# Kernel optimization log

Hardware: AMD Instinct MI355X
Metric: run time of the kernel (lower is better)

The kernel has to match this reference:

```python
import jax, jax.numpy as jnp
import numpy as np

B, D, E, K, H = 16384, 4096, 64, 8, 128


def setup_inputs() -> dict:
    key = jax.random.key(0)
    ks = jax.random.split(key, 6)
    return {
        "r_pooled": jax.random.normal(ks[0], (B, D), jnp.float32),
        "step_frac": jnp.asarray(0.37, jnp.float32),
        "hidden_norm": jax.random.uniform(ks[1], (B,), jnp.float32),
        "confidence": jax.random.uniform(ks[2], (B,), jnp.float32),
        # params stored (in, out); equivalent math to torch Linear
        "W1": jax.random.normal(ks[3], (D + 3, H), jnp.float32) / np.sqrt(D + 3),
        "b1": jnp.zeros((H,), jnp.float32),
        "W2": jax.random.normal(ks[4], (H, E), jnp.float32) / np.sqrt(H),
        "b2": jnp.zeros((E,), jnp.float32),
    }


def reference(r_pooled, step_frac, hidden_norm, confidence, W1, b1, W2, b2):
    b = r_pooled.shape[0]
    step_col = step_frac * jnp.ones((b, 1), r_pooled.dtype)  # torch.full((B,1), step_frac)
    features = jnp.concatenate(
        [r_pooled, step_col, hidden_norm[:, None], confidence[:, None]], axis=-1
    )  # (B, D+3)
    h = jax.nn.silu(features @ W1 + b1)          # (B, 128)
    logits = h @ W2 + b2                         # (B, E)
    topk_vals, topk_idx = jax.lax.top_k(logits, K)
    topk_weights = jax.nn.softmax(topk_vals, axis=-1)
    weights = jnp.zeros_like(logits).at[jnp.arange(b)[:, None], topk_idx].set(topk_weights)
    return weights, logits
```

## Files before the change

### kernel.cpp

```cpp
#include <hip/hip_runtime.h>
#include <math.h>

#define DGL 4096
#define HGL 128
#define EGL 64
#define DELTA 5e-4f

typedef short  short8 __attribute__((ext_vector_type(8)));
typedef float  f32x4  __attribute__((ext_vector_type(4)));

__device__ inline unsigned short bf16_rne(float x) {
    unsigned u = __float_as_uint(x);
    u += 0x7FFFu + ((u >> 16) & 1u);
    return (unsigned short)(u >> 16);
}
__device__ inline void split2(float x, short& hi, short& lo) {
    unsigned u = __float_as_uint(x);
    hi = (short)(u >> 16);
    float hif = __uint_as_float(u & 0xFFFF0000u);
    lo = (short)bf16_rne(x - hif);
}
__device__ inline void split8(const float* f, short8& hi, short8& lo) {
#pragma unroll
    for (int j = 0; j < 8; ++j) { short h, l2; split2(f[j], h, l2); hi[j] = h; lo[j] = l2; }
}

__global__ void pack_w1(const float* __restrict__ W1, unsigned short* __restrict__ wsB1) {
    const int b = blockIdx.x;
    const int kci = b >> 3, nt = b & 7;
    const int l = threadIdx.x, quad = l >> 4, l15 = l & 15;
    short8 vh, vl;
#pragma unroll
    for (int j = 0; j < 8; ++j) {
        const int k = kci * 32 + quad * 8 + j;
        short h, lo; split2(W1[(size_t)k * HGL + nt * 16 + l15], h, lo);
        vh[j] = h; vl[j] = lo;
    }
    *(short8*)(wsB1 + (size_t)kci * 8192 + ((nt * 2 + 0) * 64 + l) * 8) = vh;
    *(short8*)(wsB1 + (size_t)kci * 8192 + ((nt * 2 + 1) * 64 + l) * 8) = vl;
}

__global__ void pack_w2(const float* __restrict__ W2, unsigned short* __restrict__ wsB2,
                        int* __restrict__ gcount) {
    if (blockIdx.x == 0 && threadIdx.x == 0) *gcount = 0;
    const int b = blockIdx.x;
    const int kc2 = b >> 2, nt = b & 3;
    const int l = threadIdx.x, quad = l >> 4, l15 = l & 15;
    short8 vh, vl;
#pragma unroll
    for (int j = 0; j < 8; ++j) {
        const int k = kc2 * 32 + quad * 8 + j;
        short h, lo; split2(W2[k * EGL + nt * 16 + l15], h, lo);
        vh[j] = h; vl[j] = lo;
    }
    *(short8*)(wsB2 + ((kc2 * 4 + nt) * 2 + 0) * 512 + l * 8) = vh;
    *(short8*)(wsB2 + ((kc2 * 4 + nt) * 2 + 1) * 512 + l * 8) = vl;
}

__global__ __launch_bounds__(512, 2) void router_main(
    const float* __restrict__ r_pooled, const float* __restrict__ step_frac,
    const float* __restrict__ hn, const float* __restrict__ cf,
    const float* __restrict__ W1, const float* __restrict__ b1,
    const float* __restrict__ b2v,
    const unsigned short* __restrict__ wsB1, const unsigned short* __restrict__ wsB2,
    int* __restrict__ gcount, int* __restrict__ glist,
    float* __restrict__ out_w, float* __restrict__ out_l)
{
    __shared__ float hsum[32 * 132];
    __shared__ float hsum2[32 * 132];
    __shared__ float ls[32 * 65];
    __shared__ float wt[32 * 65];

    const int t = threadIdx.x;
    const int w = t >> 6, l = t & 63;
    const int quad = l >> 4, l15 = l & 15;
    const int row0 = blockIdx.x * 32;

    const float* aB0 = r_pooled + (size_t)(row0 + l15) * DGL + w * 512 + quad * 8;
    const float* aB1 = aB0 + (size_t)16 * DGL;

    f32x4 acc[2][8];
#pragma unroll
    for (int m = 0; m < 2; ++m)
#pragma unroll
        for (int nt = 0; nt < 8; ++nt) acc[m][nt] = (f32x4){0.f, 0.f, 0.f, 0.f};

    float4 a0[4];
    a0[0] = *(const float4*)(aB0);
    a0[1] = *(const float4*)(aB0 + 4);
    a0[2] = *(const float4*)(aB1);
    a0[3] = *(const float4*)(aB1 + 4);

    for (int kci = 0; kci < 16; ++kci) {
        short8 ahi[2], alo[2];
#pragma unroll
        for (int m = 0; m < 2; ++m) {
            float fa[8];
#pragma unroll
            for (int j = 0; j < 4; ++j) { fa[j] = a0[2 * m][j]; fa[j + 4] = a0[2 * m + 1][j]; }
            split8(fa, ahi[m], alo[m]);
        }
        if (kci + 1 < 16) {
            const int kn = kci + 1;
            a0[0] = *(const float4*)(aB0 + kn * 32);
            a0[1] = *(const float4*)(aB0 + kn * 32 + 4);
            a0[2] = *(const float4*)(aB1 + kn * 32);
            a0[3] = *(const float4*)(aB1 + kn * 32 + 4);
        }

        const unsigned short* bp = wsB1 + (size_t)(w * 16 + kci) * 8192 + l * 8;
        short8 bh = *(const short8*)(bp + 0 * 512);
        short8 bl = *(const short8*)(bp + 1 * 512);
#pragma unroll
        for (int nt = 0; nt < 8; ++nt) {
            short8 bhn, bln;
            if (nt < 7) {
                bhn = *(const short8*)(bp + (2 * nt + 2) * 512);
                bln = *(const short8*)(bp + (2 * nt + 3) * 512);
            }
            acc[0][nt] = __builtin_amdgcn_mfma_f32_16x16x32_bf16(ahi[0], bh, acc[0][nt], 0, 0, 0);
            acc[0][nt] = __builtin_amdgcn_mfma_f32_16x16x32_bf16(ahi[0], bl, acc[0][nt], 0, 0, 0);
            acc[0][nt] = __builtin_amdgcn_mfma_f32_16x16x32_bf16(alo[0], bh, acc[0][nt], 0, 0, 0);
            acc[1][nt] = __builtin_amdgcn_mfma_f32_16x16x32_bf16(ahi[1], bh, acc[1][nt], 0, 0, 0);
            acc[1][nt] = __builtin_amdgcn_mfma_f32_16x16x32_bf16(ahi[1], bl, acc[1][nt], 0, 0, 0);
            acc[1][nt] = __builtin_amdgcn_mfma_f32_16x16x32_bf16(alo[1], bh, acc[1][nt], 0, 0, 0);
            bh = bhn; bl = bln;
        }
    }

    if (w == 0) {
#pragma unroll
        for (int m = 0; m < 2; ++m)
#pragma unroll
            for (int nt = 0; nt < 8; ++nt)
#pragma unroll
                for (int r = 0; r < 4; ++r)
                    hsum[(m * 16 + quad * 4 + r) * 132 + nt * 16 + l15] = acc[m][nt][r];
    }
    if (w == 4) {
#pragma unroll
        for (int m = 0; m < 2; ++m)
#pragma unroll
            for (int nt = 0; nt < 8; ++nt)
#pragma unroll
                for (int r = 0; r < 4; ++r)
                    hsum2[(m * 16 + quad * 4 + r) * 132 + nt * 16 + l15] = acc[m][nt][r];
    }
    __syncthreads();
#pragma unroll
    for (int wv = 1; wv < 4; ++wv) {
        if (w == wv) {
#pragma unroll
            for (int m = 0; m < 2; ++m)
#pragma unroll
                for (int nt = 0; nt < 8; ++nt)
#pragma unroll
                    for (int r = 0; r < 4; ++r)
                        hsum[(m * 16 + quad * 4 + r) * 132 + nt * 16 + l15] += acc[m][nt][r];
        }
        if (w == wv + 4) {
#pragma unroll
            for (int m = 0; m < 2; ++m)
#pragma unroll
                for (int nt = 0; nt < 8; ++nt)
#pragma unroll
                    for (int r = 0; r < 4; ++r)
                        hsum2[(m * 16 + quad * 4 + r) * 132 + nt * 16 + l15] += acc[m][nt][r];
        }
        __syncthreads();
    }

    {
        const float sf = step_frac[0];
#pragma unroll
        for (int j = 0; j < 8; ++j) {
            const int idx = j * 512 + t;
            const int r = idx >> 7, c = idx & 127;
            float x = hsum[r * 132 + c] + hsum2[r * 132 + c];
            x += sf * W1[(size_t)4096 * HGL + c]
               + hn[row0 + r] * W1[(size_t)4097 * HGL + c]
               + cf[row0 + r] * W1[(size_t)4098 * HGL + c] + b1[c];
            hsum[r * 132 + c] = x / (1.0f + expf(-x));
        }
    }
    __syncthreads();

    const int mt2 = w >> 2, nt2 = w & 3;
    f32x4 acc2 = (f32x4){0.f, 0.f, 0.f, 0.f};
#pragma unroll
    for (int kc2 = 0; kc2 < 4; ++kc2) {
        const float4 va = *(const float4*)&hsum[(mt2 * 16 + l15) * 132 + kc2 * 32 + quad * 8];
        const float4 vb = *(const float4*)&hsum[(mt2 * 16 + l15) * 132 + kc2 * 32 + quad * 8 + 4];
        float fa[8];
#pragma unroll
        for (int j = 0; j < 4; ++j) { fa[j] = ((const float*)&va)[j]; fa[j + 4] = ((const float*)&vb)[j]; }
        short8 h2, lo2;
        split8(fa, h2, lo2);
        const short8 bh = *(const short8*)(wsB2 + ((kc2 * 4 + nt2) * 2 + 0) * 512 + l * 8);
        const short8 bl = *(const short8*)(wsB2 + ((kc2 * 4 + nt2) * 2 + 1) * 512 + l * 8);
        acc2 = __builtin_amdgcn_mfma_f32_16x16x32_bf16(h2,  bh, acc2, 0, 0, 0);
        acc2 = __builtin_amdgcn_mfma_f32_16x16x32_bf16(h2,  bl, acc2, 0, 0, 0);
        acc2 = __builtin_amdgcn_mfma_f32_16x16x32_bf16(lo2, bh, acc2, 0, 0, 0);
    }

    {
        const int c = nt2 * 16 + l15;
        const float bv = b2v[c];
#pragma unroll
        for (int r = 0; r < 4; ++r) {
            const int lr = mt2 * 16 + quad * 4 + r;
            const float v = acc2[r] + bv;
            out_l[(size_t)(row0 + lr) * EGL + c] = v;
            ls[lr * 65 + c] = v;
        }
    }
    for (int i = t; i < 32 * 65; i += 512) wt[i] = 0.0f;
    __syncthreads();

    if (t < 32) {
        float vals[9]; int idxs[9];
#pragma unroll
        for (int i = 0; i < 9; ++i) { vals[i] = -INFINITY; idxs[i] = 0; }
        for (int e = 0; e < EGL; ++e) {
            const float v = ls[t * 65 + e];
            if (v > vals[8]) {
                int p = 8;
                while (p > 0 && v > vals[p - 1]) { vals[p] = vals[p - 1]; idxs[p] = idxs[p - 1]; --p; }
                vals[p] = v; idxs[p] = e;
            }
        }
        const float mx = vals[0];
        float wgt[8], ssum = 0.0f;
#pragma unroll
        for (int i = 0; i < 8; ++i) { wgt[i] = expf(vals[i] - mx); ssum += wgt[i]; }
        const float inv = 1.0f / ssum;
#pragma unroll
        for (int i = 0; i < 8; ++i) wt[t * 65 + idxs[i]] = wgt[i] * inv;
        if (vals[7] - vals[8] < DELTA) {
            int p = atomicAdd(gcount, 1);
            if (p < 16384) glist[p] = row0 + t;
        }
    }
    __syncthreads();

    for (int i = t; i < 32 * EGL; i += 512) {
        const int m = i >> 6, c = i & 63;
        out_w[(size_t)(row0 + m) * EGL + c] = wt[m * 65 + c];
    }
}

__global__ __launch_bounds__(512, 1) void refine_rows(
    const float* __restrict__ r_pooled, const float* __restrict__ step_frac,
    const float* __restrict__ hn, const float* __restrict__ cf,
    const float* __restrict__ W1, const float* __restrict__ b1,
    const float* __restrict__ W2, const float* __restrict__ b2,
    const int* __restrict__ gcount, const int* __restrict__ glist,
    float* __restrict__ out_w)
{
    __shared__ __align__(16) float als[DGL];
    __shared__ float part[4][128];
    __shared__ float hred[128];
    __shared__ float lb[64];
    __shared__ float wb[64];

    const int t = threadIdx.x;
    const int cnt = *gcount;
    const int c = t & 127, sl = t >> 7;

    for (int i = blockIdx.x; i < cnt; i += gridDim.x) {
        const int row = glist[i];
        __syncthreads();
        for (int j = t; j < DGL / 4; j += 512)
            *(float4*)&als[j * 4] = *(const float4*)&r_pooled[(size_t)row * DGL + j * 4];
        __syncthreads();

        float pr = 0.0f;
        const float* ap = als + sl * 1024;
        const float* wp = W1 + (size_t)(sl * 1024) * HGL + c;
#pragma unroll 8
        for (int k = 0; k < 1024; ++k) pr = fmaf(ap[k], wp[(size_t)k * HGL], pr);
        part[sl][c] = pr;
        __syncthreads();

        if (t < 128) {
            const float sf = step_frac[0];
            float x = part[0][t] + part[1][t] + part[2][t] + part[3][t];
            x += sf * W1[(size_t)4096 * HGL + t] + hn[row] * W1[(size_t)4097 * HGL + t]
               + cf[row] * W1[(size_t)4098 * HGL + t] + b1[t];
            hred[t] = x / (1.0f + expf(-x));
        }
        __syncthreads();
        if (t < 64) {
            float a = b2[t];
            for (int k = 0; k < HGL; ++k) a = fmaf(hred[k], W2[k * EGL + t], a);
            lb[t] = a; wb[t] = 0.0f;
        }
        __syncthreads();
        if (t == 0) {
            float vals[8]; int idxs[8];
#pragma unroll
            for (int q = 0; q < 8; ++q) { vals[q] = -INFINITY; idxs[q] = 0; }
            for (int e = 0; e < EGL; ++e) {
                const float v = lb[e];
                if (v > vals[7]) {
                    int p = 7;
                    while (p > 0 && v > vals[p - 1]) { vals[p] = vals[p - 1]; idxs[p] = idxs[p - 1]; --p; }
                    vals[p] = v; idxs[p] = e;
                }
            }
            const float mx = vals[0];
            float wgt[8], ssum = 0.0f;
#pragma unroll
            for (int q = 0; q < 8; ++q) { wgt[q] = expf(vals[q] - mx); ssum += wgt[q]; }
            const float inv = 1.0f / ssum;
#pragma unroll
            for (int q = 0; q < 8; ++q) wb[idxs[q]] = wgt[q] * inv;
        }
        __syncthreads();
        if (t < 64) out_w[(size_t)row * EGL + t] = wb[t];
    }
}

extern "C" void kernel_launch(void* const* d_in, const int* in_sizes, int n_in,
                              void* d_out, int out_size, void* d_ws, size_t ws_size,
                              hipStream_t stream) {
    const float* r_pooled    = (const float*)d_in[0];
    const float* step_frac   = (const float*)d_in[1];
    const float* hidden_norm = (const float*)d_in[2];
    const float* confidence  = (const float*)d_in[3];
    const float* W1          = (const float*)d_in[4];
    const float* b1          = (const float*)d_in[5];
    const float* W2          = (const float*)d_in[6];
    const float* b2          = (const float*)d_in[7];

    const int B = in_sizes[2];
    float* out_w = (float*)d_out;
    float* out_l = out_w + (size_t)B * EGL;

    unsigned short* wsB1 = (unsigned short*)d_ws;
    unsigned short* wsB2 = (unsigned short*)((char*)d_ws + 2097152);
    int* gcount = (int*)((char*)d_ws + 2129920);
    int* glist  = (int*)((char*)d_ws + 2129984);

    hipLaunchKernelGGL(pack_w1, dim3(1024), dim3(64), 0, stream, W1, wsB1);
    hipLaunchKernelGGL(pack_w2, dim3(16), dim3(64), 0, stream, W2, wsB2, gcount);
    hipLaunchKernelGGL(router_main, dim3(B / 32), dim3(512), 0, stream,
                       r_pooled, step_frac, hidden_norm, confidence,
                       W1, b1, b2, wsB1, wsB2, gcount, glist, out_w, out_l);
    hipLaunchKernelGGL(refine_rows, dim3(256), dim3(512), 0, stream,
                       r_pooled, step_frac, hidden_norm, confidence,
                       W1, b1, W2, b2, gcount, glist, out_w);
}
```

Baseline: 557.2 us.

## Split waves across row halves and K quarters instead of eight K slices

Each of the 8 waves now handles one 16-row half of the 32-row tile over a quarter of K (1024), instead of both halves over an eighth of K. This halves the accumulator registers per wave and removes the second shared-memory partial-sum buffer along with its extra reduction pass. The trade-off is that each wave now reads its B fragments for only one M tile, so every wsB1 element is loaded twice per block and B-operand traffic per block doubles.

```diff
diff --git a/kernel.cpp b/kernel.cpp
--- a/kernel.cpp
+++ b/kernel.cpp
@@ -67,7 +67,6 @@
     float* __restrict__ out_w, float* __restrict__ out_l)
 {
     __shared__ float hsum[32 * 132];
-    __shared__ float hsum2[32 * 132];
     __shared__ float ls[32 * 65];
     __shared__ float wt[32 * 65];
 
@@ -76,39 +75,31 @@
     const int quad = l >> 4, l15 = l & 15;
     const int row0 = blockIdx.x * 32;
 
-    const float* aB0 = r_pooled + (size_t)(row0 + l15) * DGL + w * 512 + quad * 8;
-    const float* aB1 = aB0 + (size_t)16 * DGL;
-
-    f32x4 acc[2][8];
-#pragma unroll
-    for (int m = 0; m < 2; ++m)
-#pragma unroll
-        for (int nt = 0; nt < 8; ++nt) acc[m][nt] = (f32x4){0.f, 0.f, 0.f, 0.f};
-
-    float4 a0[4];
-    a0[0] = *(const float4*)(aB0);
-    a0[1] = *(const float4*)(aB0 + 4);
-    a0[2] = *(const float4*)(aB1);
-    a0[3] = *(const float4*)(aB1 + 4);
-
-    for (int kci = 0; kci < 16; ++kci) {
-        short8 ahi[2], alo[2];
-#pragma unroll
-        for (int m = 0; m < 2; ++m) {
+    const int kq = w & 3, mh = w >> 2;
+    const float* aB = r_pooled + (size_t)(row0 + mh * 16 + l15) * DGL + kq * 1024 + quad * 8;
+
+    f32x4 acc[8];
+#pragma unroll
+    for (int nt = 0; nt < 8; ++nt) acc[nt] = (f32x4){0.f, 0.f, 0.f, 0.f};
+
+    float4 a0[2];
+    a0[0] = *(const float4*)(aB);
+    a0[1] = *(const float4*)(aB + 4);
+
+    for (int kci = 0; kci < 32; ++kci) {
+        short8 ahi, alo;
+        {
             float fa[8];
 #pragma unroll
-            for (int j = 0; j < 4; ++j) { fa[j] = a0[2 * m][j]; fa[j + 4] = a0[2 * m + 1][j]; }
-            split8(fa, ahi[m], alo[m]);
-        }
-        if (kci + 1 < 16) {
-            const int kn = kci + 1;
-            a0[0] = *(const float4*)(aB0 + kn * 32);
-            a0[1] = *(const float4*)(aB0 + kn * 32 + 4);
-            a0[2] = *(const float4*)(aB1 + kn * 32);
-            a0[3] = *(const float4*)(aB1 + kn * 32 + 4);
-        }
-
-        const unsigned short* bp = wsB1 + (size_t)(w * 16 + kci) * 8192 + l * 8;
+            for (int j = 0; j < 4; ++j) { fa[j] = a0[0][j]; fa[j + 4] = a0[1][j]; }
+            split8(fa, ahi, alo);
+        }
+        if (kci + 1 < 32) {
+            a0[0] = *(const float4*)(aB + (kci + 1) * 32);
+            a0[1] = *(const float4*)(aB + (kci + 1) * 32 + 4);
+        }
+
+        const unsigned short* bp = wsB1 + (size_t)(kq * 32 + kci) * 8192 + l * 8;
         short8 bh = *(const short8*)(bp + 0 * 512);
         short8 bl = *(const short8*)(bp + 1 * 512);
 #pragma unroll
@@ -118,54 +109,29 @@
                 bhn = *(const short8*)(bp + (2 * nt + 2) * 512);
                 bln = *(const short8*)(bp + (2 * nt + 3) * 512);
             }
-            acc[0][nt] = __builtin_amdgcn_mfma_f32_16x16x32_bf16(ahi[0], bh, acc[0][nt], 0, 0, 0);
-            acc[0][nt] = __builtin_amdgcn_mfma_f32_16x16x32_bf16(ahi[0], bl, acc[0][nt], 0, 0, 0);
-            acc[0][nt] = __builtin_amdgcn_mfma_f32_16x16x32_bf16(alo[0], bh, acc[0][nt], 0, 0, 0);
-            acc[1][nt] = __builtin_amdgcn_mfma_f32_16x16x32_bf16(ahi[1], bh, acc[1][nt], 0, 0, 0);
-            acc[1][nt] = __builtin_amdgcn_mfma_f32_16x16x32_bf16(ahi[1], bl, acc[1][nt], 0, 0, 0);
-            acc[1][nt] = __builtin_amdgcn_mfma_f32_16x16x32_bf16(alo[1], bh, acc[1][nt], 0, 0, 0);
+            acc[nt] = __builtin_amdgcn_mfma_f32_16x16x32_bf16(ahi, bh, acc[nt], 0, 0, 0);
+            acc[nt] = __builtin_amdgcn_mfma_f32_16x16x32_bf16(ahi, bl, acc[nt], 0, 0, 0);
+            acc[nt] = __builtin_amdgcn_mfma_f32_16x16x32_bf16(alo, bh, acc[nt], 0, 0, 0);
             bh = bhn; bl = bln;
         }
     }
 
-    if (w == 0) {
-#pragma unroll
-        for (int m = 0; m < 2; ++m)
+    if (kq == 0) {
+#pragma unroll
+        for (int nt = 0; nt < 8; ++nt)
+#pragma unroll
+            for (int r = 0; r < 4; ++r)
+                hsum[(mh * 16 + quad * 4 + r) * 132 + nt * 16 + l15] = acc[nt][r];
+    }
+    __syncthreads();
+#pragma unroll
+    for (int wv = 1; wv < 4; ++wv) {
+        if (kq == wv) {
 #pragma unroll
             for (int nt = 0; nt < 8; ++nt)
 #pragma unroll
                 for (int r = 0; r < 4; ++r)
-                    hsum[(m * 16 + quad * 4 + r) * 132 + nt * 16 + l15] = acc[m][nt][r];
-    }
-    if (w == 4) {
-#pragma unroll
-        for (int m = 0; m < 2; ++m)
-#pragma unroll
-            for (int nt = 0; nt < 8; ++nt)
-#pragma unroll
-                for (int r = 0; r < 4; ++r)
-                    hsum2[(m * 16 + quad * 4 + r) * 132 + nt * 16 + l15] = acc[m][nt][r];
-    }
-    __syncthreads();
-#pragma unroll
-    for (int wv = 1; wv < 4; ++wv) {
-        if (w == wv) {
-#pragma unroll
-            for (int m = 0; m < 2; ++m)
-#pragma unroll
-                for (int nt = 0; nt < 8; ++nt)
-#pragma unroll
-                    for (int r = 0; r < 4; ++r)
-                        hsum[(m * 16 + quad * 4 + r) * 132 + nt * 16 + l15] += acc[m][nt][r];
-        }
-        if (w == wv + 4) {
-#pragma unroll
-            for (int m = 0; m < 2; ++m)
-#pragma unroll
-                for (int nt = 0; nt < 8; ++nt)
-#pragma unroll
-                    for (int r = 0; r < 4; ++r)
-                        hsum2[(m * 16 + quad * 4 + r) * 132 + nt * 16 + l15] += acc[m][nt][r];
+                    hsum[(mh * 16 + quad * 4 + r) * 132 + nt * 16 + l15] += acc[nt][r];
         }
         __syncthreads();
     }
@@ -176,7 +142,7 @@
         for (int j = 0; j < 8; ++j) {
             const int idx = j * 512 + t;
             const int r = idx >> 7, c = idx & 127;
-            float x = hsum[r * 132 + c] + hsum2[r * 132 + c];
+            float x = hsum[r * 132 + c];
             x += sf * W1[(size_t)4096 * HGL + c]
                + hn[row0 + r] * W1[(size_t)4097 * HGL + c]
                + cf[row0 + r] * W1[(size_t)4098 * HGL + c] + b1[c];
```

Result: slower. 589.5 us (+5.8%).
